# Optimization experiments

Measured on AMD Instinct MI355X. Metric: run time of the kernel, lower is better.

## Reference

```python
import jax, jax.numpy as jnp
import numpy as np

DIMS = [4096, 2048, 1024]
NUM_ITERS = 3
LR = 0.1
EPS = 1e-5


def _layer_norm(h, gamma, beta):
    mu = jnp.mean(h, axis=-1, keepdims=True)
    var = jnp.mean((h - mu) ** 2, axis=-1, keepdims=True)
    return (h - mu) * jax.lax.rsqrt(var + EPS) * gamma + beta


def _pc_layer(x, gen_w, gen_b, rec_w, rec_b, log_prec, ln_g, ln_b):
    # x: [B, in_dim]; gen_w: [in_dim, hid]; rec_w: [hid, in_dim]
    h = _layer_norm(x @ rec_w.T + rec_b, ln_g, ln_b)          # [B, hid]
    prec2 = jax.nn.softplus(log_prec) ** 2                      # [in_dim]
    for _ in range(NUM_ITERS):
        err = x - (h @ gen_w.T + gen_b)                        # [B, in_dim]
        # analytic grad of sum((err*prec)^2) wrt h is -2 * (err*prec^2) @ gen_w
        # hidden update: h - LR * grad = h + 2*LR * (err*prec2) @ gen_w
        h = _layer_norm(h + (2.0 * LR) * ((err * prec2) @ gen_w), ln_g, ln_b)
    return h


def setup_inputs() -> dict:
    key = jax.random.key(0)
    ks = jax.random.split(key, 16)
    x = jax.random.normal(ks[0], (8192, DIMS[0]), dtype=jnp.float32)
    inp = {"x": x}
    ki = 1
    for li in range(len(DIMS) - 1):
        in_d, hid = DIMS[li], DIMS[li + 1]
        inp[f"gen_w{li}"] = jax.random.normal(ks[ki], (in_d, hid), jnp.float32) / np.sqrt(hid); ki += 1
        inp[f"gen_b{li}"] = jnp.zeros((in_d,), jnp.float32)
        inp[f"rec_w{li}"] = jax.random.normal(ks[ki], (hid, in_d), jnp.float32) / np.sqrt(in_d); ki += 1
        inp[f"rec_b{li}"] = jnp.zeros((hid,), jnp.float32)
        inp[f"log_prec{li}"] = jnp.zeros((in_d,), jnp.float32)
        inp[f"ln_g{li}"] = jnp.ones((hid,), jnp.float32)
        inp[f"ln_b{li}"] = jnp.zeros((hid,), jnp.float32)
    return inp


def reference(x,
              gen_w0, gen_b0, rec_w0, rec_b0, log_prec0, ln_g0, ln_b0,
              gen_w1, gen_b1, rec_w1, rec_b1, log_prec1, ln_g1, ln_b1):
    h0 = _pc_layer(x, gen_w0, gen_b0, rec_w0, rec_b0, log_prec0, ln_g0, ln_b0)
    h1 = _pc_layer(h0, gen_w1, gen_b1, rec_w1, rec_b1, log_prec1, ln_g1, ln_b1)
    return h1
```

## Files before the change

### kernel.cpp

```cpp
#include <hip/hip_runtime.h>

typedef unsigned short u16;
using bf16x8 = __attribute__((ext_vector_type(8))) __bf16;
using f32x4  = __attribute__((ext_vector_type(4))) float;

__device__ __forceinline__ u16 f2b(float f) {
    unsigned u = __float_as_uint(f);
    u += 0x7fffu + ((u >> 16) & 1u);
    return (u16)(u >> 16);
}
__device__ __forceinline__ float b2f(u16 h) {
    return __uint_as_float(((unsigned)h) << 16);
}

__device__ __forceinline__ void gl2lds16(const void* g, void* l) {
    __builtin_amdgcn_global_load_lds(
        (const __attribute__((address_space(1))) void*)g,
        (__attribute__((address_space(3))) void*)l, 16, 0, 0);
}

__global__ __launch_bounds__(256) void cast_bf16_kernel(
        const float4* __restrict__ src, ushort4* __restrict__ dst, int n4) {
    int i = blockIdx.x * 256 + threadIdx.x;
    if (i < n4) {
        float4 v = src[i];
        ushort4 o; o.x = f2b(v.x); o.y = f2b(v.y); o.z = f2b(v.z); o.w = f2b(v.w);
        dst[i] = o;
    }
}

__global__ __launch_bounds__(256) void prec2_kernel(
        const float* __restrict__ lp, float* __restrict__ p2, int n) {
    int i = blockIdx.x * 256 + threadIdx.x;
    if (i < n) {
        float v = lp[i];
        float sp = fmaxf(v, 0.f) + log1pf(expf(-fabsf(v)));
        p2[i] = sp * sp;
    }
}

__global__ __launch_bounds__(256) void transpose_cast_kernel(
        const float* __restrict__ src, u16* __restrict__ dst, int R, int C,
        const float* __restrict__ scale) {
    __shared__ float tile[32][33];
    const int bx = blockIdx.x * 32;
    const int by = blockIdx.y * 32;
    const int tx = threadIdx.x & 31;
    const int ty = threadIdx.x >> 5;
#pragma unroll
    for (int i = 0; i < 32; i += 8) {
        float s = scale ? scale[by + ty + i] : 1.f;
        tile[ty + i][tx] = s * src[(size_t)(by + ty + i) * C + (bx + tx)];
    }
    __syncthreads();
#pragma unroll
    for (int i = 0; i < 32; i += 8)
        dst[(size_t)(bx + ty + i) * R + (by + tx)] = f2b(tile[tx][ty + i]);
}

__global__ __launch_bounds__(256) void cvec_kernel(
        const float* __restrict__ gb, const u16* __restrict__ DGt,
        float* __restrict__ cv, int in) {
    const int j = blockIdx.x * 4 + (threadIdx.x >> 6);
    const int lane = threadIdx.x & 63;
    const u16* row = DGt + (size_t)j * in;
    float s = 0.f;
    for (int i = lane; i < in; i += 64) s += gb[i] * b2f(row[i]);
#pragma unroll
    for (int off = 32; off > 0; off >>= 1) s += __shfl_down(s, off);
    if (lane == 0) cv[j] = s;
}

template <int F32OUT>
__global__ __launch_bounds__(256) void ln_kernel(
        const float* __restrict__ T, const float* __restrict__ g,
        const float* __restrict__ b, void* __restrict__ outp, int D) {
    const int row = blockIdx.x;
    const int tid = threadIdx.x;
    const int nv  = D >> 2;
    const float4* rp = (const float4*)(T + (size_t)row * D);

    float4 vals[2];
    float s = 0.f, sq = 0.f;
    int cnt = 0;
    for (int i = tid; i < nv; i += 256) {
        float4 v = rp[i];
        vals[cnt++] = v;
        s  += v.x + v.y + v.z + v.w;
        sq += v.x * v.x + v.y * v.y + v.z * v.z + v.w * v.w;
    }
#pragma unroll
    for (int off = 32; off > 0; off >>= 1) {
        s  += __shfl_down(s, off);
        sq += __shfl_down(sq, off);
    }
    __shared__ float ssum[4], ssq[4];
    if ((tid & 63) == 0) { ssum[tid >> 6] = s; ssq[tid >> 6] = sq; }
    __syncthreads();
    const float ts = ssum[0] + ssum[1] + ssum[2] + ssum[3];
    const float tq = ssq[0] + ssq[1] + ssq[2] + ssq[3];
    const float mu   = ts / (float)D;
    const float rstd = rsqrtf(tq / (float)D - mu * mu + 1e-5f);

    cnt = 0;
    for (int i = tid; i < nv; i += 256) {
        float4 v  = vals[cnt++];
        float4 gg = ((const float4*)g)[i];
        float4 bb = ((const float4*)b)[i];
        float o0 = (v.x - mu) * rstd * gg.x + bb.x;
        float o1 = (v.y - mu) * rstd * gg.y + bb.y;
        float o2 = (v.z - mu) * rstd * gg.z + bb.z;
        float o3 = (v.w - mu) * rstd * gg.w + bb.w;
        if (F32OUT) {
            ((float4*)outp)[(size_t)row * nv + i] = make_float4(o0, o1, o2, o3);
        } else {
            ushort4 o; o.x = f2b(o0); o.y = f2b(o1); o.z = f2b(o2); o.w = f2b(o3);
            ((ushort4*)outp)[(size_t)row * nv + i] = o;
        }
    }
}

enum { EPI_BIAS = 0, EPI_CMB = 1, EPI_W = 2, EPI_ITER = 3 };

template <int EPI>
__global__ __launch_bounds__(256) void gemm_bt(
        const u16* __restrict__ A, const u16* __restrict__ Bt, int N, int K,
        const float* __restrict__ bias, const u16* __restrict__ Cc,
        const u16* __restrict__ H, void* __restrict__ outp) {
    __shared__ u16 As[128 * 32];
    __shared__ u16 Bs[128 * 32];

    const int tid  = threadIdx.x;
    const int lane = tid & 63;
    const int wave = tid >> 6;
    const size_t row0 = (size_t)blockIdx.y * 128;
    const size_t col0 = (size_t)blockIdx.x * 128;

    const int sr = tid >> 2;
    const int sc = (tid & 3) * 8;
    const u16* gA0 = A  + (row0 + sr) * K + sc;
    const u16* gA1 = gA0 + (size_t)64 * K;
    const u16* gB0 = Bt + (col0 + sr) * K + sc;
    const u16* gB1 = gB0 + (size_t)64 * K;
    char* lA = (char*)As + wave * 1024;
    char* lB = (char*)Bs + wave * 1024;

    const int wm = wave >> 1, wn = wave & 1;
    const int fr = lane & 15;
    const int fq = lane >> 4;
    const bf16x8* aP[4];
    const bf16x8* bP[4];
#pragma unroll
    for (int i = 0; i < 4; ++i) {
        aP[i] = (const bf16x8*)(As + (wm * 64 + i * 16 + fr) * 32 + fq * 8);
        bP[i] = (const bf16x8*)(Bs + (wn * 64 + i * 16 + fr) * 32 + fq * 8);
    }

    f32x4 acc[4][4];
    const f32x4 zero = {0.f, 0.f, 0.f, 0.f};
#pragma unroll
    for (int i = 0; i < 4; ++i)
#pragma unroll
        for (int j = 0; j < 4; ++j) acc[i][j] = zero;

    for (int k0 = 0; k0 < K; k0 += 32) {
        __syncthreads();
        gl2lds16(gA0, lA);
        gl2lds16(gA1, lA + 4096);
        gl2lds16(gB0, lB);
        gl2lds16(gB1, lB + 4096);
        __syncthreads();
        bf16x8 af[4], bfr[4];
#pragma unroll
        for (int i = 0; i < 4; ++i) { af[i] = *aP[i]; bfr[i] = *bP[i]; }
#pragma unroll
        for (int i = 0; i < 4; ++i)
#pragma unroll
            for (int j = 0; j < 4; ++j)
                acc[i][j] = __builtin_amdgcn_mfma_f32_16x16x32_bf16(
                    af[i], bfr[j], acc[i][j], 0, 0, 0);
        gA0 += 32; gA1 += 32; gB0 += 32; gB1 += 32;
    }

#pragma unroll
    for (int i = 0; i < 4; ++i) {
#pragma unroll
        for (int r = 0; r < 4; ++r) {
            const size_t gr = row0 + wm * 64 + i * 16 + fq * 4 + r;
#pragma unroll
            for (int j = 0; j < 4; ++j) {
                const size_t gc  = col0 + wn * 64 + j * 16 + fr;
                const size_t idx = gr * (size_t)N + gc;
                const float v = acc[i][j][r];
                if (EPI == EPI_BIAS) {
                    ((float*)outp)[idx] = v + bias[gc];
                } else if (EPI == EPI_CMB) {
                    ((u16*)outp)[idx] = f2b(v - bias[gc]);
                } else if (EPI == EPI_W) {
                    ((u16*)outp)[idx] = f2b(v);
                } else {
                    ((float*)outp)[idx] = b2f(H[idx]) + 0.2f * (b2f(Cc[idx]) - v);
                }
            }
        }
    }
}

template <int EPI>
__global__ __launch_bounds__(512, 2) void gemm256(
        const u16* __restrict__ A, const u16* __restrict__ Bt, int N, int K,
        const float* __restrict__ bias, const u16* __restrict__ Cc,
        const u16* __restrict__ H, void* __restrict__ outp) {
    extern __shared__ char smem[];

    const int tid  = threadIdx.x;
    const int lane = tid & 63;
    const int w    = tid >> 6;
    const int wm   = w >> 2;
    const int wn   = w & 3;
    const int fr   = lane & 15;
    const int fq   = lane >> 4;

    const int nwg = gridDim.x * gridDim.y;
    const int bid = blockIdx.y * gridDim.x + blockIdx.x;
    int sbid = bid;
    if (!(nwg & 7)) sbid = (bid & 7) * (nwg >> 3) + (bid >> 3);
    const int bx = sbid % gridDim.x;
    const int by = sbid / gridDim.x;
    const size_t row0 = (size_t)by * 256;
    const size_t col0 = (size_t)bx * 256;

    const int scol = ((lane & 7) ^ (lane >> 3)) << 4;
    const char* sA[2][2];
    const char* sB[2][2];
    int dA[2][2], dB[2][2];
#pragma unroll
    for (int h = 0; h < 2; ++h)
#pragma unroll
        for (int g = 0; g < 2; ++g) {
            const size_t rr = (size_t)(h * 128 + g * 64 + w * 8 + (lane >> 3));
            sA[h][g] = (const char*)A  + (row0 + rr) * (size_t)K * 2 + scol;
            sB[h][g] = (const char*)Bt + (col0 + rr) * (size_t)K * 2 + scol;
            dA[h][g] = h * 16384 + (g * 64 + w * 8) * 128;
            dB[h][g] = 32768 + dA[h][g];
        }

    const int swzR = (fr & 7) << 4;
    int aoff[2], boff[2];
#pragma unroll
    for (int s = 0; s < 2; ++s) {
        aoff[s] = ((fr * 128 + s * 64 + fq * 16) ^ swzR) + wm * 16384;
        boff[s] = ((((wn & 1) * 64 + fr) * 128 + s * 64 + fq * 16) ^ swzR)
                  + 32768 + (wn >> 1) * 16384;
    }

    f32x4 acc[8][4];
    const f32x4 zero = {0.f, 0.f, 0.f, 0.f};
#pragma unroll
    for (int i = 0; i < 8; ++i)
#pragma unroll
        for (int j = 0; j < 4; ++j) acc[i][j] = zero;

#pragma unroll
    for (int h = 0; h < 2; ++h)
#pragma unroll
        for (int g = 0; g < 2; ++g) {
            gl2lds16(sA[h][g], smem + dA[h][g]);
            gl2lds16(sB[h][g], smem + dB[h][g]);
        }
    __builtin_amdgcn_sched_barrier(0);
#pragma unroll
    for (int h = 0; h < 2; ++h)
#pragma unroll
        for (int g = 0; g < 2; ++g) {
            gl2lds16(sA[h][g] + 128, smem + 65536 + dA[h][g]);
            gl2lds16(sB[h][g] + 128, smem + 65536 + dB[h][g]);
        }
    asm volatile("s_waitcnt vmcnt(8)");
    __builtin_amdgcn_sched_barrier(0);
    __builtin_amdgcn_s_barrier();
    __builtin_amdgcn_sched_barrier(0);

    const int T = K >> 6;
    for (int t = 0; t < T; ++t) {
        const char* base = smem + ((t & 1) << 16);
        const int kb = (t + 2) * 128;
        bf16x8 a[8][2], b[4][2];

#pragma unroll
        for (int i = 0; i < 4; ++i)
#pragma unroll
            for (int s = 0; s < 2; ++s)
                a[i][s] = *(const bf16x8*)(base + aoff[s] + i * 2048);
#pragma unroll
        for (int j = 0; j < 2; ++j)
#pragma unroll
            for (int s = 0; s < 2; ++s)
                b[j][s] = *(const bf16x8*)(base + boff[s] + j * 2048);
#pragma unroll
        for (int i = 4; i < 8; ++i)
#pragma unroll
            for (int s = 0; s < 2; ++s)
                a[i][s] = *(const bf16x8*)(base + aoff[s] + i * 2048);
#pragma unroll
        for (int j = 2; j < 4; ++j)
#pragma unroll
            for (int s = 0; s < 2; ++s)
                b[j][s] = *(const bf16x8*)(base + boff[s] + j * 2048);
        __builtin_amdgcn_sched_barrier(0);
        __builtin_amdgcn_s_barrier();
        __builtin_amdgcn_sched_barrier(0);

        asm volatile("s_waitcnt lgkmcnt(12)");
        __builtin_amdgcn_sched_barrier(0);
        __builtin_amdgcn_s_setprio(1);
#pragma unroll
        for (int i = 0; i < 4; ++i)
#pragma unroll
            for (int j = 0; j < 2; ++j)
#pragma unroll
                for (int s = 0; s < 2; ++s)
                    acc[i][j] = __builtin_amdgcn_mfma_f32_16x16x32_bf16(
                        a[i][s], b[j][s], acc[i][j], 0, 0, 0);
        __builtin_amdgcn_s_setprio(0);
        __builtin_amdgcn_sched_barrier(0);
        __builtin_amdgcn_s_barrier();
        __builtin_amdgcn_sched_barrier(0);

        asm volatile("s_waitcnt lgkmcnt(4)");
        __builtin_amdgcn_sched_barrier(0);
        __builtin_amdgcn_s_setprio(1);
#pragma unroll
        for (int i = 4; i < 8; ++i)
#pragma unroll
            for (int j = 0; j < 2; ++j)
#pragma unroll
                for (int s = 0; s < 2; ++s)
                    acc[i][j] = __builtin_amdgcn_mfma_f32_16x16x32_bf16(
                        a[i][s], b[j][s], acc[i][j], 0, 0, 0);
        __builtin_amdgcn_s_setprio(0);
        __builtin_amdgcn_sched_barrier(0);
        __builtin_amdgcn_s_barrier();
        __builtin_amdgcn_sched_barrier(0);

        if (t + 2 < T) {
#pragma unroll
            for (int h = 0; h < 2; ++h)
#pragma unroll
                for (int g = 0; g < 2; ++g)
                    gl2lds16(sA[h][g] + kb, smem + ((t & 1) << 16) + dA[h][g]);
        }
        __builtin_amdgcn_sched_barrier(0);
        asm volatile("s_waitcnt lgkmcnt(0)");
        __builtin_amdgcn_sched_barrier(0);
        __builtin_amdgcn_s_setprio(1);
#pragma unroll
        for (int i = 0; i < 4; ++i)
#pragma unroll
            for (int j = 2; j < 4; ++j)
#pragma unroll
                for (int s = 0; s < 2; ++s)
                    acc[i][j] = __builtin_amdgcn_mfma_f32_16x16x32_bf16(
                        a[i][s], b[j][s], acc[i][j], 0, 0, 0);
        __builtin_amdgcn_s_setprio(0);
        __builtin_amdgcn_sched_barrier(0);
        __builtin_amdgcn_s_barrier();
        __builtin_amdgcn_sched_barrier(0);

        if (t + 2 < T) {
#pragma unroll
            for (int h = 0; h < 2; ++h)
#pragma unroll
                for (int g = 0; g < 2; ++g)
                    gl2lds16(sB[h][g] + kb, smem + ((t & 1) << 16) + dB[h][g]);
        }
        __builtin_amdgcn_sched_barrier(0);
        __builtin_amdgcn_s_setprio(1);
#pragma unroll
        for (int i = 4; i < 8; ++i)
#pragma unroll
            for (int j = 2; j < 4; ++j)
#pragma unroll
                for (int s = 0; s < 2; ++s)
                    acc[i][j] = __builtin_amdgcn_mfma_f32_16x16x32_bf16(
                        a[i][s], b[j][s], acc[i][j], 0, 0, 0);
        __builtin_amdgcn_s_setprio(0);
        __builtin_amdgcn_sched_barrier(0);
        if (t + 2 < T) {
            asm volatile("s_waitcnt vmcnt(6)");
        } else if (t + 2 == T) {
            asm volatile("s_waitcnt vmcnt(0)");
        }
        __builtin_amdgcn_sched_barrier(0);
        __builtin_amdgcn_s_barrier();
        __builtin_amdgcn_sched_barrier(0);
    }

#pragma unroll
    for (int i = 0; i < 8; ++i) {
#pragma unroll
        for (int r = 0; r < 4; ++r) {
            const size_t gr = row0 + wm * 128 + i * 16 + fq * 4 + r;
#pragma unroll
            for (int j = 0; j < 4; ++j) {
                const size_t gc  = col0 + wn * 64 + j * 16 + fr;
                const size_t idx = gr * (size_t)N + gc;
                const float v = acc[i][j][r];
                if (EPI == EPI_BIAS) {
                    ((float*)outp)[idx] = v + bias[gc];
                } else if (EPI == EPI_CMB) {
                    ((u16*)outp)[idx] = f2b(v - bias[gc]);
                } else if (EPI == EPI_W) {
                    ((u16*)outp)[idx] = f2b(v);
                } else {
                    ((float*)outp)[idx] = b2f(H[idx]) + 0.2f * (b2f(Cc[idx]) - v);
                }
            }
        }
    }
}

extern "C" void kernel_launch(void* const* d_in, const int* in_sizes, int n_in,
                              void* d_out, int out_size, void* d_ws, size_t ws_size,
                              hipStream_t stream) {
    const int B = 8192;
    const float* x      = (const float*)d_in[0];
    const float* gen_w0 = (const float*)d_in[1];
    const float* gen_b0 = (const float*)d_in[2];
    const float* rec_w0 = (const float*)d_in[3];
    const float* rec_b0 = (const float*)d_in[4];
    const float* log_p0 = (const float*)d_in[5];
    const float* ln_g0  = (const float*)d_in[6];
    const float* ln_b0  = (const float*)d_in[7];
    const float* gen_w1 = (const float*)d_in[8];
    const float* gen_b1 = (const float*)d_in[9];
    const float* rec_w1 = (const float*)d_in[10];
    const float* rec_b1 = (const float*)d_in[11];
    const float* log_p1 = (const float*)d_in[12];
    const float* ln_g1  = (const float*)d_in[13];
    const float* ln_b1  = (const float*)d_in[14];

    char* ws = (char*)d_ws;
    auto alloc = [&](size_t bytes) -> char* {
        char* p = ws;
        ws += (bytes + 255) & ~(size_t)255;
        return p;
    };
    u16*   Xb   = (u16*)  alloc((size_t)B * 4096 * 2);
    float* Tf   = (float*)alloc((size_t)B * 2048 * 4);
    u16*   Hb0  = (u16*)  alloc((size_t)B * 2048 * 2);
    u16*   Cb0  = (u16*)  alloc((size_t)B * 2048 * 2);
    u16*   rwb0 = (u16*)  alloc((size_t)2048 * 4096 * 2);
    u16*   DGt0 = (u16*)  alloc((size_t)2048 * 4096 * 2);
    u16*   W0   = (u16*)  alloc((size_t)2048 * 2048 * 2);
    float* p20  = (float*)alloc(4096 * 4);
    float* p21  = (float*)alloc(2048 * 4);
    float* cv0  = (float*)alloc(2048 * 4);
    float* cv1  = (float*)alloc(1024 * 4);

    u16* Gt0 = Cb0;
    u16* Hb1 = DGt0;
    char* l1 = (char*)Xb;
    u16* rwb1 = (u16*)l1;                 l1 += (size_t)1024 * 2048 * 2;
    u16* Gt1  = (u16*)l1;                 l1 += (size_t)1024 * 2048 * 2;
    u16* DGt1 = (u16*)l1;                 l1 += (size_t)1024 * 2048 * 2;
    u16* W1   = (u16*)l1;                 l1 += (size_t)1024 * 1024 * 2;
    u16* Cb1  = (u16*)l1;                 l1 += (size_t)B * 1024 * 2;

    auto cast = [&](const float* s, u16* d, size_t n) {
        int n4 = (int)(n >> 2);
        cast_bf16_kernel<<<dim3((n4 + 255) / 256), dim3(256), 0, stream>>>(
            (const float4*)s, (ushort4*)d, n4);
    };
    const dim3 blk(256);
    const dim3 blk8(512);
    const size_t LDS8 = 131072;

    prec2_kernel<<<dim3(16), blk, 0, stream>>>(log_p0, p20, 4096);
    prec2_kernel<<<dim3(8),  blk, 0, stream>>>(log_p1, p21, 2048);
    cast(x, Xb, (size_t)B * 4096);
    cast(rec_w0, rwb0, (size_t)2048 * 4096);
    transpose_cast_kernel<<<dim3(2048 / 32, 4096 / 32), blk, 0, stream>>>(
        gen_w0, Gt0, 4096, 2048, nullptr);
    transpose_cast_kernel<<<dim3(2048 / 32, 4096 / 32), blk, 0, stream>>>(
        gen_w0, DGt0, 4096, 2048, p20);
    cvec_kernel<<<dim3(2048 / 4), blk, 0, stream>>>(gen_b0, DGt0, cv0, 4096);
    gemm_bt<EPI_W><<<dim3(16, 16), blk, 0, stream>>>(
        Gt0, DGt0, 2048, 4096, nullptr, nullptr, nullptr, W0);

    gemm256<EPI_BIAS><<<dim3(8, 32), blk8, LDS8, stream>>>(
        Xb, rwb0, 2048, 4096, rec_b0, nullptr, nullptr, Tf);
    ln_kernel<0><<<dim3(B), blk, 0, stream>>>(Tf, ln_g0, ln_b0, Hb0, 2048);
    gemm256<EPI_CMB><<<dim3(8, 32), blk8, LDS8, stream>>>(
        Xb, DGt0, 2048, 4096, cv0, nullptr, nullptr, Cb0);

    cast(rec_w1, rwb1, (size_t)1024 * 2048);
    transpose_cast_kernel<<<dim3(1024 / 32, 2048 / 32), blk, 0, stream>>>(
        gen_w1, Gt1, 2048, 1024, nullptr);
    transpose_cast_kernel<<<dim3(1024 / 32, 2048 / 32), blk, 0, stream>>>(
        gen_w1, DGt1, 2048, 1024, p21);
    cvec_kernel<<<dim3(1024 / 4), blk, 0, stream>>>(gen_b1, DGt1, cv1, 2048);
    gemm_bt<EPI_W><<<dim3(8, 8), blk, 0, stream>>>(
        Gt1, DGt1, 1024, 2048, nullptr, nullptr, nullptr, W1);

    for (int it = 0; it < 3; ++it) {
        gemm256<EPI_ITER><<<dim3(8, 32), blk8, LDS8, stream>>>(
            Hb0, W0, 2048, 2048, nullptr, Cb0, Hb0, Tf);
        ln_kernel<0><<<dim3(B), blk, 0, stream>>>(Tf, ln_g0, ln_b0, Hb0, 2048);
    }

    gemm256<EPI_BIAS><<<dim3(4, 32), blk8, LDS8, stream>>>(
        Hb0, rwb1, 1024, 2048, rec_b1, nullptr, nullptr, Tf);
    ln_kernel<0><<<dim3(B), blk, 0, stream>>>(Tf, ln_g1, ln_b1, Hb1, 1024);
    gemm256<EPI_CMB><<<dim3(4, 32), blk8, LDS8, stream>>>(
        Hb0, DGt1, 1024, 2048, cv1, nullptr, nullptr, Cb1);
    for (int it = 0; it < 3; ++it) {
        gemm256<EPI_ITER><<<dim3(4, 32), blk8, LDS8, stream>>>(
            Hb1, W1, 1024, 1024, nullptr, Cb1, Hb1, Tf);
        if (it < 2)
            ln_kernel<0><<<dim3(B), blk, 0, stream>>>(Tf, ln_g1, ln_b1, Hb1, 1024);
        else
            ln_kernel<1><<<dim3(B), blk, 0, stream>>>(Tf, ln_g1, ln_b1, d_out, 1024);
    }
}
```

Measured before the change: 1.467 ms.

## Restructure gemm256 LDS pipeline and use smaller-tile GEMM for layer 1

Rewrites the main loop of the 256-tile GEMM so the second halves of the A and B fragments are read from LDS just before the MFMA groups that use them, not all up front. It also cuts the barriers from four to two per iteration and replaces the sched_barrier and lgkmcnt fences with vmcnt waits that carry memory clobbers. Separately, the layer-1 GEMMs (N=1024) switch to the smaller-tile gemm_bt kernel with more blocks, to occupy more CUs on the narrower problem. The looser synchronisation risks LDS read/write races, and the compiler may now reorder the loads and MFMAs.

```diff
diff --git a/kernel.cpp b/kernel.cpp
--- a/kernel.cpp
+++ b/kernel.cpp
@@ -268,7 +268,6 @@
             gl2lds16(sA[h][g], smem + dA[h][g]);
             gl2lds16(sB[h][g], smem + dB[h][g]);
         }
-    __builtin_amdgcn_sched_barrier(0);
 #pragma unroll
     for (int h = 0; h < 2; ++h)
 #pragma unroll
@@ -276,10 +275,8 @@
             gl2lds16(sA[h][g] + 128, smem + 65536 + dA[h][g]);
             gl2lds16(sB[h][g] + 128, smem + 65536 + dB[h][g]);
         }
-    asm volatile("s_waitcnt vmcnt(8)");
-    __builtin_amdgcn_sched_barrier(0);
+    asm volatile("s_waitcnt vmcnt(8)" ::: "memory");
     __builtin_amdgcn_s_barrier();
-    __builtin_amdgcn_sched_barrier(0);
 
     const int T = K >> 6;
     for (int t = 0; t < T; ++t) {
@@ -297,22 +294,6 @@
 #pragma unroll
             for (int s = 0; s < 2; ++s)
                 b[j][s] = *(const bf16x8*)(base + boff[s] + j * 2048);
-#pragma unroll
-        for (int i = 4; i < 8; ++i)
-#pragma unroll
-            for (int s = 0; s < 2; ++s)
-                a[i][s] = *(const bf16x8*)(base + aoff[s] + i * 2048);
-#pragma unroll
-        for (int j = 2; j < 4; ++j)
-#pragma unroll
-            for (int s = 0; s < 2; ++s)
-                b[j][s] = *(const bf16x8*)(base + boff[s] + j * 2048);
-        __builtin_amdgcn_sched_barrier(0);
-        __builtin_amdgcn_s_barrier();
-        __builtin_amdgcn_sched_barrier(0);
-
-        asm volatile("s_waitcnt lgkmcnt(12)");
-        __builtin_amdgcn_sched_barrier(0);
         __builtin_amdgcn_s_setprio(1);
 #pragma unroll
         for (int i = 0; i < 4; ++i)
@@ -323,12 +304,12 @@
                     acc[i][j] = __builtin_amdgcn_mfma_f32_16x16x32_bf16(
                         a[i][s], b[j][s], acc[i][j], 0, 0, 0);
         __builtin_amdgcn_s_setprio(0);
-        __builtin_amdgcn_sched_barrier(0);
-        __builtin_amdgcn_s_barrier();
-        __builtin_amdgcn_sched_barrier(0);
-
-        asm volatile("s_waitcnt lgkmcnt(4)");
-        __builtin_amdgcn_sched_barrier(0);
+
+#pragma unroll
+        for (int i = 4; i < 8; ++i)
+#pragma unroll
+            for (int s = 0; s < 2; ++s)
+                a[i][s] = *(const bf16x8*)(base + aoff[s] + i * 2048);
         __builtin_amdgcn_s_setprio(1);
 #pragma unroll
         for (int i = 4; i < 8; ++i)
@@ -339,9 +320,8 @@
                     acc[i][j] = __builtin_amdgcn_mfma_f32_16x16x32_bf16(
                         a[i][s], b[j][s], acc[i][j], 0, 0, 0);
         __builtin_amdgcn_s_setprio(0);
-        __builtin_amdgcn_sched_barrier(0);
+        asm volatile("s_waitcnt vmcnt(4)" ::: "memory");
         __builtin_amdgcn_s_barrier();
-        __builtin_amdgcn_sched_barrier(0);
 
         if (t + 2 < T) {
 #pragma unroll
@@ -350,9 +330,11 @@
                 for (int g = 0; g < 2; ++g)
                     gl2lds16(sA[h][g] + kb, smem + ((t & 1) << 16) + dA[h][g]);
         }
-        __builtin_amdgcn_sched_barrier(0);
-        asm volatile("s_waitcnt lgkmcnt(0)");
-        __builtin_amdgcn_sched_barrier(0);
+#pragma unroll
+        for (int j = 2; j < 4; ++j)
+#pragma unroll
+            for (int s = 0; s < 2; ++s)
+                b[j][s] = *(const bf16x8*)(base + boff[s] + j * 2048);
         __builtin_amdgcn_s_setprio(1);
 #pragma unroll
         for (int i = 0; i < 4; ++i)
@@ -363,9 +345,12 @@
                     acc[i][j] = __builtin_amdgcn_mfma_f32_16x16x32_bf16(
                         a[i][s], b[j][s], acc[i][j], 0, 0, 0);
         __builtin_amdgcn_s_setprio(0);
-        __builtin_amdgcn_sched_barrier(0);
+        if (t + 2 < T) {
+            asm volatile("s_waitcnt vmcnt(4)" ::: "memory");
+        } else {
+            asm volatile("s_waitcnt vmcnt(0)" ::: "memory");
+        }
         __builtin_amdgcn_s_barrier();
-        __builtin_amdgcn_sched_barrier(0);
 
         if (t + 2 < T) {
 #pragma unroll
@@ -374,7 +359,6 @@
                 for (int g = 0; g < 2; ++g)
                     gl2lds16(sB[h][g] + kb, smem + ((t & 1) << 16) + dB[h][g]);
         }
-        __builtin_amdgcn_sched_barrier(0);
         __builtin_amdgcn_s_setprio(1);
 #pragma unroll
         for (int i = 4; i < 8; ++i)
@@ -385,15 +369,6 @@
                     acc[i][j] = __builtin_amdgcn_mfma_f32_16x16x32_bf16(
                         a[i][s], b[j][s], acc[i][j], 0, 0, 0);
         __builtin_amdgcn_s_setprio(0);
-        __builtin_amdgcn_sched_barrier(0);
-        if (t + 2 < T) {
-            asm volatile("s_waitcnt vmcnt(6)");
-        } else if (t + 2 == T) {
-            asm volatile("s_waitcnt vmcnt(0)");
-        }
-        __builtin_amdgcn_sched_barrier(0);
-        __builtin_amdgcn_s_barrier();
-        __builtin_amdgcn_sched_barrier(0);
     }
 
 #pragma unroll
@@ -509,13 +484,13 @@
         ln_kernel<0><<<dim3(B), blk, 0, stream>>>(Tf, ln_g0, ln_b0, Hb0, 2048);
     }
 
-    gemm256<EPI_BIAS><<<dim3(4, 32), blk8, LDS8, stream>>>(
+    gemm_bt<EPI_BIAS><<<dim3(8, 64), blk, 0, stream>>>(
         Hb0, rwb1, 1024, 2048, rec_b1, nullptr, nullptr, Tf);
     ln_kernel<0><<<dim3(B), blk, 0, stream>>>(Tf, ln_g1, ln_b1, Hb1, 1024);
-    gemm256<EPI_CMB><<<dim3(4, 32), blk8, LDS8, stream>>>(
+    gemm_bt<EPI_CMB><<<dim3(8, 64), blk, 0, stream>>>(
         Hb0, DGt1, 1024, 2048, cv1, nullptr, nullptr, Cb1);
     for (int it = 0; it < 3; ++it) {
-        gemm256<EPI_ITER><<<dim3(4, 32), blk8, LDS8, stream>>>(
+        gemm_bt<EPI_ITER><<<dim3(8, 64), blk, 0, stream>>>(
             Hb1, W1, 1024, 1024, nullptr, Cb1, Hb1, Tf);
         if (it < 2)
             ln_kernel<0><<<dim3(B), blk, 0, stream>>>(Tf, ln_g1, ln_b1, Hb1, 1024);
```

After: 1.319 ms. 10.0% less time.
